# Kernel optimization log

Hardware: AMD Instinct MI355X
Metric: run time of the kernel (lower is better)

The kernel has to match this reference:

```python
import jax, jax.numpy as jnp
import numpy as np

N_NODES = 50000
N_EDGES = 800000


def gcn_conv(x, edge_index, W, b):
    """PyG GCNConv: add self-loops, symmetric deg^{-1/2} normalization,
    dense transform, scatter-add aggregation."""
    n = x.shape[0]
    src, dst = edge_index[0], edge_index[1]
    # add self-loops
    loop = jnp.arange(n, dtype=src.dtype)
    src = jnp.concatenate([src, loop])
    dst = jnp.concatenate([dst, loop])
    # degree on destination nodes (includes self-loops -> deg >= 1)
    deg = jax.ops.segment_sum(jnp.ones_like(dst, dtype=x.dtype), dst, num_segments=n)
    dinv = jax.lax.rsqrt(deg)
    norm = dinv[src] * dinv[dst]  # [E+N]
    h = x @ W                     # [N, F_out] dense GEMM
    msg = h[src] * norm[:, None]  # gather + scale, [E+N, F_out]
    out = jax.ops.segment_sum(msg, dst, num_segments=n)  # scatter-add
    return out + b


def setup_inputs() -> dict:
    key = jax.random.key(0)
    ks = jax.random.split(key, 8)
    x = jax.random.normal(ks[0], (N_NODES, 100), dtype=jnp.float32)
    edge_index = jax.random.randint(ks[1], (2, N_EDGES), 0, N_NODES, dtype=jnp.int64)
    W1 = jax.random.normal(ks[2], (100, 256), dtype=jnp.float32) * 0.1
    b1 = jnp.zeros((256,), dtype=jnp.float32)
    W2 = jax.random.normal(ks[3], (256, 128), dtype=jnp.float32) * 0.06
    b2 = jnp.zeros((128,), dtype=jnp.float32)
    Wfc = jax.random.normal(ks[4], (128, 1), dtype=jnp.float32) * 0.09
    bfc = jnp.zeros((1,), dtype=jnp.float32)
    return {"x": x, "edge_index": edge_index, "W1": W1, "b1": b1,
            "W2": W2, "b2": b2, "Wfc": Wfc, "bfc": bfc}


def reference(x, edge_index, W1, b1, W2, b2, Wfc, bfc):
    # eval mode: F.dropout with training=False is identity
    h = jax.nn.relu(gcn_conv(x, edge_index, W1, b1))
    h = jax.nn.relu(gcn_conv(h, edge_index, W2, b2))
    return h @ Wfc + bfc  # [N, 1]
```

## Files before the change

### kernel.cpp

```cpp
#include <hip/hip_runtime.h>
#include <hip/hip_bf16.h>


#define F0 100
#define F1 256
#define F2 128
#define CAP 2048

typedef _Float16 f16x4 __attribute__((ext_vector_type(4)));
typedef _Float16 f16x8 __attribute__((ext_vector_type(8)));
typedef float f32x4 __attribute__((ext_vector_type(4)));


__global__ void zero_i32(int* p, int n) {
    int i = blockIdx.x * blockDim.x + threadIdx.x;
    if (i < n) p[i] = 0;
}

__global__ void fill_f32(float* out, const float* __restrict__ bfc, int n) {
    int i = blockIdx.x * blockDim.x + threadIdx.x;
    if (i < n) out[i] = bfc[0];
}

__global__ void deg_count_i(const int* __restrict__ dst, int* deg, int e) {
    int i = blockIdx.x * blockDim.x + threadIdx.x;
    if (i < e) atomicAdd(deg + dst[i], 1);
}

__global__ __launch_bounds__(256) void scan1(const int* __restrict__ deg,
                                             int* __restrict__ excl,
                                             int* __restrict__ bsum,
                                             float* __restrict__ dinv, int n) {
    __shared__ int wsum[4];
    int i = blockIdx.x * 256 + threadIdx.x;
    int lane = threadIdx.x & 63, wid = threadIdx.x >> 6;
    int v = (i < n) ? deg[i] : 0;
    if (i < n) dinv[i] = rsqrtf((float)(v + 1));
    int s = v;
#pragma unroll
    for (int off = 1; off < 64; off <<= 1) {
        int t = __shfl_up(s, off, 64);
        if (lane >= off) s += t;
    }
    if (lane == 63) wsum[wid] = s;
    __syncthreads();
    int add = 0;
    for (int w = 0; w < wid; w++) add += wsum[w];
    if (i < n) excl[i] = add + s - v;
    if (threadIdx.x == 255) bsum[blockIdx.x] = add + s;
}

__global__ __launch_bounds__(256) void scan2(int* __restrict__ bsum, int nb,
                                             int* __restrict__ rowptr, int n) {
    __shared__ int wsum[4];
    int lane = threadIdx.x & 63, wid = threadIdx.x >> 6;
    int v = (threadIdx.x < nb) ? bsum[threadIdx.x] : 0;
    int s = v;
#pragma unroll
    for (int off = 1; off < 64; off <<= 1) {
        int t = __shfl_up(s, off, 64);
        if (lane >= off) s += t;
    }
    if (lane == 63) wsum[wid] = s;
    __syncthreads();
    int add = 0;
    for (int w = 0; w < wid; w++) add += wsum[w];
    if (threadIdx.x < nb) bsum[threadIdx.x] = add + s - v;
    if (threadIdx.x == 255) rowptr[n] = add + s;
}

__global__ void scan3(const int* __restrict__ excl, const int* __restrict__ bsum,
                      int* __restrict__ rowptr, int* __restrict__ cursor, int n) {
    int i = blockIdx.x * 256 + threadIdx.x;
    if (i < n) {
        int r = excl[i] + bsum[blockIdx.x];
        rowptr[i] = r;
        cursor[i] = r;
    }
}

__global__ void csr_fill(const int* __restrict__ src, const int* __restrict__ dst,
                         int* cursor, int* __restrict__ csr, int e) {
    int i = blockIdx.x * blockDim.x + threadIdx.x;
    if (i < e) {
        int pos = atomicAdd(cursor + dst[i], 1);
        csr[pos] = src[i];
    }
}

__global__ void scale_x(const float4* __restrict__ x4,
                        const float* __restrict__ dinv,
                        float4* __restrict__ xs4, int n25) {
    int i = blockIdx.x * blockDim.x + threadIdx.x;
    if (i < n25) {
        float d = dinv[i / 25];
        float4 v = x4[i];
        v.x *= d; v.y *= d; v.z *= d; v.w *= d;
        xs4[i] = v;
    }
}

__global__ void wprep(const float* __restrict__ W1, const float* __restrict__ W2,
                      _Float16* __restrict__ W1h, _Float16* __restrict__ W1l,
                      _Float16* __restrict__ W2h, _Float16* __restrict__ W2l) {
    int i = blockIdx.x * 256 + threadIdx.x;
    if (i < 256 * 128) {
        int c = i >> 7, k = i & 127;
        float v = (k < F0) ? W1[(size_t)k * F1 + c] : 0.f;
        _Float16 h = (_Float16)v;
        W1h[i] = h;
        W1l[i] = (_Float16)(v - (float)h);
    } else if (i < 256 * 128 + 128 * 256) {
        int j = i - 256 * 128;
        int c = j >> 8, k = j & 255;
        float v = W2[(size_t)k * F2 + c];
        _Float16 h = (_Float16)v;
        W2h[j] = h;
        W2l[j] = (_Float16)(v - (float)h);
    }
}


__global__ __launch_bounds__(256) void pull_f100(
        const float* __restrict__ xs, const int* __restrict__ rowptr,
        const int* __restrict__ csr, const float* __restrict__ dinv,
        _Float16* __restrict__ aggh, _Float16* __restrict__ aggl, int n) {
    int wave = threadIdx.x >> 6, lane = threadIdx.x & 63;
    int v = blockIdx.x * 4 + wave;
    if (v >= n) return;
    int beg = rowptr[v], end = rowptr[v + 1];
    float dv = dinv[v];
    int half = lane >> 5, q = lane & 31;
    bool act = q < 25;
    float4 acc = {0.f, 0.f, 0.f, 0.f};
    if (half == 0 && act) acc = ((const float4*)(xs + (size_t)v * F0))[q];

    for (int base = beg; base < end; base += 64) {
        int cnt = min(64, end - base);
        int sidx = (lane < cnt) ? csr[base + lane] : 0;
        int npf = cnt >> 1;
        int p = 0;
        for (; p + 4 <= npf; p += 4) {
            int s0 = __shfl(sidx, 2 * p + half, 64);
            int s1 = __shfl(sidx, 2 * p + 2 + half, 64);
            int s2 = __shfl(sidx, 2 * p + 4 + half, 64);
            int s3 = __shfl(sidx, 2 * p + 6 + half, 64);
            if (act) {
                float4 r0 = ((const float4*)(xs + (size_t)s0 * F0))[q];
                float4 r1 = ((const float4*)(xs + (size_t)s1 * F0))[q];
                float4 r2 = ((const float4*)(xs + (size_t)s2 * F0))[q];
                float4 r3 = ((const float4*)(xs + (size_t)s3 * F0))[q];
                acc.x += (r0.x + r1.x) + (r2.x + r3.x);
                acc.y += (r0.y + r1.y) + (r2.y + r3.y);
                acc.z += (r0.z + r1.z) + (r2.z + r3.z);
                acc.w += (r0.w + r1.w) + (r2.w + r3.w);
            }
        }
        for (; p < npf; p++) {
            int s0 = __shfl(sidx, 2 * p + half, 64);
            if (act) {
                float4 r0 = ((const float4*)(xs + (size_t)s0 * F0))[q];
                acc.x += r0.x; acc.y += r0.y; acc.z += r0.z; acc.w += r0.w;
            }
        }
        if (cnt & 1) {
            int sl = __shfl(sidx, cnt - 1, 64);
            if (half == 0 && act) {
                float4 r = ((const float4*)(xs + (size_t)sl * F0))[q];
                acc.x += r.x; acc.y += r.y; acc.z += r.z; acc.w += r.w;
            }
        }
    }
    float ox = __shfl_down(acc.x, 32, 64);
    float oy = __shfl_down(acc.y, 32, 64);
    float oz = __shfl_down(acc.z, 32, 64);
    float ow = __shfl_down(acc.w, 32, 64);
    if (half == 0) {
        float4 r = {0.f, 0.f, 0.f, 0.f};
        if (act) {
            r.x = dv * (acc.x + ox);
            r.y = dv * (acc.y + oy);
            r.z = dv * (acc.z + oz);
            r.w = dv * (acc.w + ow);
        }
        f16x4 hh, ll;
        hh[0] = (_Float16)r.x; ll[0] = (_Float16)(r.x - (float)hh[0]);
        hh[1] = (_Float16)r.y; ll[1] = (_Float16)(r.y - (float)hh[1]);
        hh[2] = (_Float16)r.z; ll[2] = (_Float16)(r.z - (float)hh[2]);
        hh[3] = (_Float16)r.w; ll[3] = (_Float16)(r.w - (float)hh[3]);
        *(f16x4*)(aggh + (size_t)v * 128 + 4 * q) = hh;
        *(f16x4*)(aggl + (size_t)v * 128 + 4 * q) = ll;
    }
}


__global__ __launch_bounds__(256) void gemm1_mfma(
        const _Float16* __restrict__ Ah, const _Float16* __restrict__ Al,
        const _Float16* __restrict__ Bh, const _Float16* __restrict__ Bl,
        const float* __restrict__ bias,
        _Float16* __restrict__ Ch, _Float16* __restrict__ Cl, int n) {
    __shared__ _Float16 sAh[128][40], sAl[128][40], sBh[128][40], sBl[128][40];
    int tid = threadIdx.x, lane = tid & 63, wave = tid >> 6;
    int wm = wave >> 1, wn = wave & 1;
    int r0 = blockIdx.x * 128, c0 = blockIdx.y * 128;
    int lr = lane & 15, ks8 = (lane >> 4) * 8;
    f32x4 acc[4][4] = {};

    for (int k0 = 0; k0 < 128; k0 += 32) {
        if (k0) __syncthreads();
#pragma unroll
        for (int p = 0; p < 2; ++p) {
            int u = tid + p * 256;
            int row = u >> 2, vv = u & 3;
            int gr = min(r0 + row, n - 1);
            *(f16x8*)&sAh[row][vv * 8] = *(const f16x8*)(Ah + (size_t)gr * 128 + k0 + vv * 8);
            *(f16x8*)&sAl[row][vv * 8] = *(const f16x8*)(Al + (size_t)gr * 128 + k0 + vv * 8);
            *(f16x8*)&sBh[row][vv * 8] = *(const f16x8*)(Bh + (size_t)(c0 + row) * 128 + k0 + vv * 8);
            *(f16x8*)&sBl[row][vv * 8] = *(const f16x8*)(Bl + (size_t)(c0 + row) * 128 + k0 + vv * 8);
        }
        __syncthreads();
        f16x8 a_h[4], a_l[4], b_h[4], b_l[4];
#pragma unroll
        for (int f = 0; f < 4; ++f) {
            a_h[f] = *(const f16x8*)&sAh[wm * 64 + f * 16 + lr][ks8];
            a_l[f] = *(const f16x8*)&sAl[wm * 64 + f * 16 + lr][ks8];
            b_h[f] = *(const f16x8*)&sBh[wn * 64 + f * 16 + lr][ks8];
            b_l[f] = *(const f16x8*)&sBl[wn * 64 + f * 16 + lr][ks8];
        }
#pragma unroll
        for (int i = 0; i < 4; ++i)
#pragma unroll
            for (int j = 0; j < 4; ++j) {
                acc[i][j] = __builtin_amdgcn_mfma_f32_16x16x32_f16(a_l[i], b_h[j], acc[i][j], 0, 0, 0);
                acc[i][j] = __builtin_amdgcn_mfma_f32_16x16x32_f16(a_h[i], b_l[j], acc[i][j], 0, 0, 0);
                acc[i][j] = __builtin_amdgcn_mfma_f32_16x16x32_f16(a_h[i], b_h[j], acc[i][j], 0, 0, 0);
            }
    }
#pragma unroll
    for (int j = 0; j < 4; ++j) {
        int col = c0 + wn * 64 + j * 16 + lr;
        float bv = bias[col];
#pragma unroll
        for (int i = 0; i < 4; ++i) {
            int rbase = r0 + wm * 64 + i * 16 + (lane >> 4) * 4;
#pragma unroll
            for (int r = 0; r < 4; ++r) {
                int gr = rbase + r;
                if (gr < n) {
                    float vv = fmaxf(acc[i][j][r] + bv, 0.f);
                    _Float16 h = (_Float16)vv;
                    Ch[(size_t)gr * 256 + col] = h;
                    Cl[(size_t)gr * 256 + col] = (_Float16)(vv - (float)h);
                }
            }
        }
    }
}

__global__ __launch_bounds__(256) void gemm2_mfma(
        const _Float16* __restrict__ Ah, const _Float16* __restrict__ Al,
        const _Float16* __restrict__ Bh, const _Float16* __restrict__ Bl,
        const float* __restrict__ dinv, float* __restrict__ C, int n) {
    __shared__ _Float16 sAh[128][40], sAl[128][40], sBh[128][40], sBl[128][40];
    int tid = threadIdx.x, lane = tid & 63, wave = tid >> 6;
    int wm = wave >> 1, wn = wave & 1;
    int r0 = blockIdx.x * 128;
    int lr = lane & 15, ks8 = (lane >> 4) * 8;
    f32x4 acc[4][4] = {};

    for (int k0 = 0; k0 < 256; k0 += 32) {
        if (k0) __syncthreads();
#pragma unroll
        for (int p = 0; p < 2; ++p) {
            int u = tid + p * 256;
            int row = u >> 2, vv = u & 3;
            int gr = min(r0 + row, n - 1);
            *(f16x8*)&sAh[row][vv * 8] = *(const f16x8*)(Ah + (size_t)gr * 256 + k0 + vv * 8);
            *(f16x8*)&sAl[row][vv * 8] = *(const f16x8*)(Al + (size_t)gr * 256 + k0 + vv * 8);
            *(f16x8*)&sBh[row][vv * 8] = *(const f16x8*)(Bh + (size_t)row * 256 + k0 + vv * 8);
            *(f16x8*)&sBl[row][vv * 8] = *(const f16x8*)(Bl + (size_t)row * 256 + k0 + vv * 8);
        }
        __syncthreads();
        f16x8 a_h[4], a_l[4], b_h[4], b_l[4];
#pragma unroll
        for (int f = 0; f < 4; ++f) {
            a_h[f] = *(const f16x8*)&sAh[wm * 64 + f * 16 + lr][ks8];
            a_l[f] = *(const f16x8*)&sAl[wm * 64 + f * 16 + lr][ks8];
            b_h[f] = *(const f16x8*)&sBh[wn * 64 + f * 16 + lr][ks8];
            b_l[f] = *(const f16x8*)&sBl[wn * 64 + f * 16 + lr][ks8];
        }
#pragma unroll
        for (int i = 0; i < 4; ++i)
#pragma unroll
            for (int j = 0; j < 4; ++j) {
                acc[i][j] = __builtin_amdgcn_mfma_f32_16x16x32_f16(a_l[i], b_h[j], acc[i][j], 0, 0, 0);
                acc[i][j] = __builtin_amdgcn_mfma_f32_16x16x32_f16(a_h[i], b_l[j], acc[i][j], 0, 0, 0);
                acc[i][j] = __builtin_amdgcn_mfma_f32_16x16x32_f16(a_h[i], b_h[j], acc[i][j], 0, 0, 0);
            }
    }
#pragma unroll
    for (int j = 0; j < 4; ++j) {
        int chunk = wn * 4 + j;
#pragma unroll
        for (int i = 0; i < 4; ++i) {
            int rbase = r0 + wm * 64 + i * 16 + (lane >> 4) * 4;
#pragma unroll
            for (int r = 0; r < 4; ++r) {
                int gr = rbase + r;
                if (gr < n) {
                    float d = dinv[gr];
                    C[((size_t)chunk * n + gr) * 16 + lr] = acc[i][j][r] * d;
                }
            }
        }
    }
}


__global__ __launch_bounds__(256) void pull_c16_fused(
        const float* __restrict__ h2c, const int* __restrict__ rowptr,
        const int* __restrict__ csr, const float* __restrict__ dinv,
        const float* __restrict__ b2, const float* __restrict__ Wfc,
        float* __restrict__ out, int n) {
    __shared__ int s_row[65];
    __shared__ float s_dinv[64];
    __shared__ int s_csr[CAP];
    int chunk = blockIdx.x & 7;
    int nb = blockIdx.x >> 3;
    int v0 = nb * 64;
    int tid = threadIdx.x;
    int lane = tid & 63, wv = tid >> 6;
    int q = lane & 3;
    int g2 = (lane >> 2) & 3;
    int grp = lane >> 4;
    const float* __restrict__ tab = h2c + (size_t)chunk * n * 16;

    if (tid <= 64) s_row[tid] = rowptr[min(v0 + tid, n)];
    if (tid < 64) s_dinv[tid] = (v0 + tid < n) ? dinv[v0 + tid] : 0.f;
    __syncthreads();
    int ebeg = s_row[0], eend = s_row[64];

    int base_local = wv * 16 + grp * 4;

    float4 acc[4];
#pragma unroll
    for (int nn = 0; nn < 4; ++nn) acc[nn] = (float4){0.f, 0.f, 0.f, 0.f};

#pragma unroll
    for (int nn = 0; nn < 4; ++nn) {
        int node = v0 + base_local + nn;
        if (node < n && g2 == 0)
            acc[nn] = ((const float4*)(tab + (size_t)node * 16))[q];
    }

    for (int w0 = ebeg; w0 < eend; w0 += CAP) {
        int wcnt = min(CAP, eend - w0);
        if (w0 != ebeg) __syncthreads();
        for (int i = tid; i < wcnt; i += 256)
            s_csr[i] = __builtin_nontemporal_load(csr + w0 + i);
        __syncthreads();
#pragma unroll
        for (int nn = 0; nn < 4; ++nn) {
            int local = base_local + nn;
            int nbg = max(s_row[local], w0) - w0;
            int nen = min(s_row[local + 1], w0 + wcnt) - w0;
            for (int t = nbg + 4 * g2; t < nen; t += 16) {
                int i1 = min(t + 1, nen - 1);
                int i2 = min(t + 2, nen - 1);
                int i3 = min(t + 3, nen - 1);
                int s0 = s_csr[t];
                int s1 = s_csr[i1];
                int s2 = s_csr[i2];
                int s3 = s_csr[i3];
                float4 r0 = ((const float4*)(tab + (size_t)s0 * 16))[q];
                float4 r1 = ((const float4*)(tab + (size_t)s1 * 16))[q];
                float4 r2 = ((const float4*)(tab + (size_t)s2 * 16))[q];
                float4 r3 = ((const float4*)(tab + (size_t)s3 * 16))[q];
                bool m1 = (t + 1 < nen), m2 = (t + 2 < nen), m3 = (t + 3 < nen);
                acc[nn].x += r0.x + (m1 ? r1.x : 0.f);
                acc[nn].y += r0.y + (m1 ? r1.y : 0.f);
                acc[nn].z += r0.z + (m1 ? r1.z : 0.f);
                acc[nn].w += r0.w + (m1 ? r1.w : 0.f);
                acc[nn].x += (m2 ? r2.x : 0.f) + (m3 ? r3.x : 0.f);
                acc[nn].y += (m2 ? r2.y : 0.f) + (m3 ? r3.y : 0.f);
                acc[nn].z += (m2 ? r2.z : 0.f) + (m3 ? r3.z : 0.f);
                acc[nn].w += (m2 ? r2.w : 0.f) + (m3 ? r3.w : 0.f);
            }
        }
    }

    int c0 = chunk * 16 + 4 * q;
    float4 bb = *(const float4*)(b2 + c0);
    float4 ww = *(const float4*)(Wfc + c0);
#pragma unroll
    for (int nn = 0; nn < 4; ++nn) {
        int local = base_local + nn;
        int node = v0 + local;
        float dv = s_dinv[local];
        float4 a = acc[nn];
        a.x += __shfl_xor(a.x, 4, 64);
        a.y += __shfl_xor(a.y, 4, 64);
        a.z += __shfl_xor(a.z, 4, 64);
        a.w += __shfl_xor(a.w, 4, 64);
        a.x += __shfl_xor(a.x, 8, 64);
        a.y += __shfl_xor(a.y, 8, 64);
        a.z += __shfl_xor(a.z, 8, 64);
        a.w += __shfl_xor(a.w, 8, 64);
        float part = fmaxf(fmaf(dv, a.x, bb.x), 0.f) * ww.x
                   + fmaxf(fmaf(dv, a.y, bb.y), 0.f) * ww.y
                   + fmaxf(fmaf(dv, a.z, bb.z), 0.f) * ww.z
                   + fmaxf(fmaf(dv, a.w, bb.w), 0.f) * ww.w;
        part += __shfl_xor(part, 1, 64);
        part += __shfl_xor(part, 2, 64);
        if (node < n && (lane & 15) == 0) atomicAdd(out + node, part);
    }
}


extern "C" void kernel_launch(void* const* d_in, const int* in_sizes, int n_in,
                              void* d_out, int out_size, void* d_ws, size_t ws_size,
                              hipStream_t stream) {
    const float* x   = (const float*)d_in[0];
    const int*   ei  = (const int*)d_in[1];
    const float* W1  = (const float*)d_in[2];
    const float* b1  = (const float*)d_in[3];
    const float* W2  = (const float*)d_in[4];
    const float* b2  = (const float*)d_in[5];
    const float* Wfc = (const float*)d_in[6];
    const float* bfc = (const float*)d_in[7];
    float* out = (float*)d_out;

    const int n = in_sizes[0] / F0;
    const int e = in_sizes[1] / 2;
    const int* src = ei;
    const int* dst = ei + e;

    char* wsb = (char*)d_ws;
    size_t off = 0;
    auto alloc = [&](size_t bytes) -> void* {
        off = (off + 255) & ~(size_t)255;
        void* r = wsb + off;
        off += bytes;
        return r;
    };
    int* deg    = (int*)alloc((size_t)n * 4);
    int* excl   = (int*)alloc((size_t)n * 4);
    int* bsum   = (int*)alloc(1024);
    int* rowptr = (int*)alloc((size_t)(n + 1) * 4);
    int* cursor = (int*)alloc((size_t)n * 4);
    int* csr    = (int*)alloc((size_t)e * 4);
    float* dinv = (float*)alloc((size_t)n * 4);
    _Float16* W1h = (_Float16*)alloc(256 * 128 * 2);
    _Float16* W1l = (_Float16*)alloc(256 * 128 * 2);
    _Float16* W2h = (_Float16*)alloc(128 * 256 * 2);
    _Float16* W2l = (_Float16*)alloc(128 * 256 * 2);
    char* bufA = (char*)alloc((size_t)n * 256 * 2 * 2);
    float* xs = (float*)bufA;
    _Float16* a1h = (_Float16*)bufA;
    _Float16* a1l = a1h + (size_t)n * 256;
    char* bufB = (char*)alloc((size_t)n * 128 * 4);
    _Float16* aggh = (_Float16*)bufB;
    _Float16* aggl = aggh + (size_t)n * 128;
    float* h2c = (float*)bufB;

    const int B = 256;
    const int nb = (n + B - 1) / B;
    const int rblocks = (n + 127) / 128;

    zero_i32<<<nb, B, 0, stream>>>(deg, n);
    fill_f32<<<nb, B, 0, stream>>>(out, bfc, n);
    deg_count_i<<<(e + B - 1) / B, B, 0, stream>>>(dst, deg, e);
    scan1<<<nb, B, 0, stream>>>(deg, excl, bsum, dinv, n);
    scale_x<<<((n * 25) + B - 1) / B, B, 0, stream>>>(
        (const float4*)x, dinv, (float4*)xs, n * 25);
    wprep<<<256, 256, 0, stream>>>(W1, W2, W1h, W1l, W2h, W2l);
    scan2<<<1, B, 0, stream>>>(bsum, nb, rowptr, n);
    scan3<<<nb, B, 0, stream>>>(excl, bsum, rowptr, cursor, n);
    csr_fill<<<(e + B - 1) / B, B, 0, stream>>>(src, dst, cursor, csr, e);

    pull_f100<<<(n + 3) / 4, 256, 0, stream>>>(xs, rowptr, csr, dinv, aggh, aggl, n);
    gemm1_mfma<<<dim3(rblocks, 2), 256, 0, stream>>>(aggh, aggl, W1h, W1l, b1,
                                                     a1h, a1l, n);
    gemm2_mfma<<<rblocks, 256, 0, stream>>>(a1h, a1l, W2h, W2l, dinv, h2c, n);
    pull_c16_fused<<<8 * ((n + 63) / 64), 256, 0, stream>>>(
        h2c, rowptr, csr, dinv, b2, Wfc, out, n);
}
```

Measured before the change: 346.6 us.

## Fuse layer-1 and layer-2 GEMMs into one kernel keeping hidden tile in LDS

Merges the two MFMA GEMMs into a single 512-thread kernel. Each block computes its 128-row slice of the 256-wide hidden activation in registers, applies bias and ReLU, and stages the split-fp16 result in LDS in two halves, which feed the second GEMM directly. This removes the global write and re-read of the n×256 hi/lo intermediate and one launch. The first GEMM now reads A and W1 straight from global memory without LDS staging, and the two-half staging adds barriers. The grid shrinks to one block per 128 rows (about 391 blocks of 512 threads), and the large register and LDS footprint may cut occupancy.

```diff
diff --git a/kernel.cpp b/kernel.cpp
--- a/kernel.cpp
+++ b/kernel.cpp
@@ -193,127 +193,117 @@
     }
 }
 
-
-__global__ __launch_bounds__(256) void gemm1_mfma(
+__global__ __launch_bounds__(512) void gemm12_fused(
         const _Float16* __restrict__ Ah, const _Float16* __restrict__ Al,
-        const _Float16* __restrict__ Bh, const _Float16* __restrict__ Bl,
-        const float* __restrict__ bias,
-        _Float16* __restrict__ Ch, _Float16* __restrict__ Cl, int n) {
-    __shared__ _Float16 sAh[128][40], sAl[128][40], sBh[128][40], sBl[128][40];
+        const _Float16* __restrict__ W1h, const _Float16* __restrict__ W1l,
+        const _Float16* __restrict__ W2h, const _Float16* __restrict__ W2l,
+        const float* __restrict__ b1, const float* __restrict__ dinv,
+        float* __restrict__ C, int n) {
+    __shared__ _Float16 sAh[128][136], sAl[128][136];
     int tid = threadIdx.x, lane = tid & 63, wave = tid >> 6;
-    int wm = wave >> 1, wn = wave & 1;
-    int r0 = blockIdx.x * 128, c0 = blockIdx.y * 128;
-    int lr = lane & 15, ks8 = (lane >> 4) * 8;
-    f32x4 acc[4][4] = {};
-
+    int wm = wave >> 2, wn = wave & 3;
+    int r0 = blockIdx.x * 128;
+    int lr = lane & 15, kg = lane >> 4, ks8 = kg * 8;
+
+    f32x4 acc1[4][4] = {};
+    int arow[4];
+#pragma unroll
+    for (int i = 0; i < 4; ++i) arow[i] = min(r0 + wm * 64 + i * 16 + lr, n - 1);
+
+#pragma unroll
     for (int k0 = 0; k0 < 128; k0 += 32) {
-        if (k0) __syncthreads();
-#pragma unroll
-        for (int p = 0; p < 2; ++p) {
-            int u = tid + p * 256;
-            int row = u >> 2, vv = u & 3;
-            int gr = min(r0 + row, n - 1);
-            *(f16x8*)&sAh[row][vv * 8] = *(const f16x8*)(Ah + (size_t)gr * 128 + k0 + vv * 8);
-            *(f16x8*)&sAl[row][vv * 8] = *(const f16x8*)(Al + (size_t)gr * 128 + k0 + vv * 8);
-            *(f16x8*)&sBh[row][vv * 8] = *(const f16x8*)(Bh + (size_t)(c0 + row) * 128 + k0 + vv * 8);
-            *(f16x8*)&sBl[row][vv * 8] = *(const f16x8*)(Bl + (size_t)(c0 + row) * 128 + k0 + vv * 8);
+        f16x8 a_h[4], a_l[4], b_h[4], b_l[4];
+#pragma unroll
+        for (int i = 0; i < 4; ++i) {
+            a_h[i] = *(const f16x8*)(Ah + (size_t)arow[i] * 128 + k0 + ks8);
+            a_l[i] = *(const f16x8*)(Al + (size_t)arow[i] * 128 + k0 + ks8);
+        }
+#pragma unroll
+        for (int j = 0; j < 4; ++j) {
+            int col = wn * 64 + j * 16 + lr;
+            b_h[j] = *(const f16x8*)(W1h + (size_t)col * 128 + k0 + ks8);
+            b_l[j] = *(const f16x8*)(W1l + (size_t)col * 128 + k0 + ks8);
+        }
+#pragma unroll
+        for (int i = 0; i < 4; ++i)
+#pragma unroll
+            for (int j = 0; j < 4; ++j) {
+                acc1[i][j] = __builtin_amdgcn_mfma_f32_16x16x32_f16(a_l[i], b_h[j], acc1[i][j], 0, 0, 0);
+                acc1[i][j] = __builtin_amdgcn_mfma_f32_16x16x32_f16(a_h[i], b_l[j], acc1[i][j], 0, 0, 0);
+                acc1[i][j] = __builtin_amdgcn_mfma_f32_16x16x32_f16(a_h[i], b_h[j], acc1[i][j], 0, 0, 0);
+            }
+    }
+#pragma unroll
+    for (int j = 0; j < 4; ++j) {
+        float bv = b1[wn * 64 + j * 16 + lr];
+#pragma unroll
+        for (int i = 0; i < 4; ++i)
+#pragma unroll
+            for (int r = 0; r < 4; ++r)
+                acc1[i][j][r] = fmaxf(acc1[i][j][r] + bv, 0.f);
+    }
+
+    f32x4 acc2[4][2] = {};
+#pragma unroll
+    for (int half = 0; half < 2; ++half) {
+        if (half) __syncthreads();
+        if ((wn >> 1) == half) {
+            int cb = (wn & 1) * 64;
+#pragma unroll
+            for (int i = 0; i < 4; ++i)
+#pragma unroll
+                for (int j = 0; j < 4; ++j)
+#pragma unroll
+                    for (int r = 0; r < 4; ++r) {
+                        int row = wm * 64 + i * 16 + kg * 4 + r;
+                        int col = cb + j * 16 + lr;
+                        float v = acc1[i][j][r];
+                        _Float16 h = (_Float16)v;
+                        sAh[row][col] = h;
+                        sAl[row][col] = (_Float16)(v - (float)h);
+                    }
         }
         __syncthreads();
-        f16x8 a_h[4], a_l[4], b_h[4], b_l[4];
-#pragma unroll
-        for (int f = 0; f < 4; ++f) {
-            a_h[f] = *(const f16x8*)&sAh[wm * 64 + f * 16 + lr][ks8];
-            a_l[f] = *(const f16x8*)&sAl[wm * 64 + f * 16 + lr][ks8];
-            b_h[f] = *(const f16x8*)&sBh[wn * 64 + f * 16 + lr][ks8];
-            b_l[f] = *(const f16x8*)&sBl[wn * 64 + f * 16 + lr][ks8];
-        }
-#pragma unroll
-        for (int i = 0; i < 4; ++i)
-#pragma unroll
-            for (int j = 0; j < 4; ++j) {
-                acc[i][j] = __builtin_amdgcn_mfma_f32_16x16x32_f16(a_l[i], b_h[j], acc[i][j], 0, 0, 0);
-                acc[i][j] = __builtin_amdgcn_mfma_f32_16x16x32_f16(a_h[i], b_l[j], acc[i][j], 0, 0, 0);
-                acc[i][j] = __builtin_amdgcn_mfma_f32_16x16x32_f16(a_h[i], b_h[j], acc[i][j], 0, 0, 0);
-            }
-    }
-#pragma unroll
-    for (int j = 0; j < 4; ++j) {
-        int col = c0 + wn * 64 + j * 16 + lr;
-        float bv = bias[col];
-#pragma unroll
-        for (int i = 0; i < 4; ++i) {
-            int rbase = r0 + wm * 64 + i * 16 + (lane >> 4) * 4;
-#pragma unroll
-            for (int r = 0; r < 4; ++r) {
-                int gr = rbase + r;
-                if (gr < n) {
-                    float vv = fmaxf(acc[i][j][r] + bv, 0.f);
-                    _Float16 h = (_Float16)vv;
-                    Ch[(size_t)gr * 256 + col] = h;
-                    Cl[(size_t)gr * 256 + col] = (_Float16)(vv - (float)h);
+#pragma unroll
+        for (int k0 = 0; k0 < 128; k0 += 32) {
+            f16x8 a_h[4], a_l[4], b_h[2], b_l[2];
+#pragma unroll
+            for (int i = 0; i < 4; ++i) {
+                a_h[i] = *(const f16x8*)&sAh[wm * 64 + i * 16 + lr][k0 + ks8];
+                a_l[i] = *(const f16x8*)&sAl[wm * 64 + i * 16 + lr][k0 + ks8];
+            }
+#pragma unroll
+            for (int j = 0; j < 2; ++j) {
+                int col = wn * 32 + j * 16 + lr;
+                int kk = half * 128 + k0 + ks8;
+                b_h[j] = *(const f16x8*)(W2h + (size_t)col * 256 + kk);
+                b_l[j] = *(const f16x8*)(W2l + (size_t)col * 256 + kk);
+            }
+#pragma unroll
+            for (int i = 0; i < 4; ++i)
+#pragma unroll
+                for (int j = 0; j < 2; ++j) {
+                    acc2[i][j] = __builtin_amdgcn_mfma_f32_16x16x32_f16(a_l[i], b_h[j], acc2[i][j], 0, 0, 0);
+                    acc2[i][j] = __builtin_amdgcn_mfma_f32_16x16x32_f16(a_h[i], b_l[j], acc2[i][j], 0, 0, 0);
+                    acc2[i][j] = __builtin_amdgcn_mfma_f32_16x16x32_f16(a_h[i], b_h[j], acc2[i][j], 0, 0, 0);
                 }
-            }
-        }
-    }
-}
-
-__global__ __launch_bounds__(256) void gemm2_mfma(
-        const _Float16* __restrict__ Ah, const _Float16* __restrict__ Al,
-        const _Float16* __restrict__ Bh, const _Float16* __restrict__ Bl,
-        const float* __restrict__ dinv, float* __restrict__ C, int n) {
-    __shared__ _Float16 sAh[128][40], sAl[128][40], sBh[128][40], sBl[128][40];
-    int tid = threadIdx.x, lane = tid & 63, wave = tid >> 6;
-    int wm = wave >> 1, wn = wave & 1;
-    int r0 = blockIdx.x * 128;
-    int lr = lane & 15, ks8 = (lane >> 4) * 8;
-    f32x4 acc[4][4] = {};
-
-    for (int k0 = 0; k0 < 256; k0 += 32) {
-        if (k0) __syncthreads();
-#pragma unroll
-        for (int p = 0; p < 2; ++p) {
-            int u = tid + p * 256;
-            int row = u >> 2, vv = u & 3;
-            int gr = min(r0 + row, n - 1);
-            *(f16x8*)&sAh[row][vv * 8] = *(const f16x8*)(Ah + (size_t)gr * 256 + k0 + vv * 8);
-            *(f16x8*)&sAl[row][vv * 8] = *(const f16x8*)(Al + (size_t)gr * 256 + k0 + vv * 8);
-            *(f16x8*)&sBh[row][vv * 8] = *(const f16x8*)(Bh + (size_t)row * 256 + k0 + vv * 8);
-            *(f16x8*)&sBl[row][vv * 8] = *(const f16x8*)(Bl + (size_t)row * 256 + k0 + vv * 8);
-        }
-        __syncthreads();
-        f16x8 a_h[4], a_l[4], b_h[4], b_l[4];
-#pragma unroll
-        for (int f = 0; f < 4; ++f) {
-            a_h[f] = *(const f16x8*)&sAh[wm * 64 + f * 16 + lr][ks8];
-            a_l[f] = *(const f16x8*)&sAl[wm * 64 + f * 16 + lr][ks8];
-            b_h[f] = *(const f16x8*)&sBh[wn * 64 + f * 16 + lr][ks8];
-            b_l[f] = *(const f16x8*)&sBl[wn * 64 + f * 16 + lr][ks8];
-        }
-#pragma unroll
-        for (int i = 0; i < 4; ++i)
-#pragma unroll
-            for (int j = 0; j < 4; ++j) {
-                acc[i][j] = __builtin_amdgcn_mfma_f32_16x16x32_f16(a_l[i], b_h[j], acc[i][j], 0, 0, 0);
-                acc[i][j] = __builtin_amdgcn_mfma_f32_16x16x32_f16(a_h[i], b_l[j], acc[i][j], 0, 0, 0);
-                acc[i][j] = __builtin_amdgcn_mfma_f32_16x16x32_f16(a_h[i], b_h[j], acc[i][j], 0, 0, 0);
-            }
-    }
-#pragma unroll
-    for (int j = 0; j < 4; ++j) {
-        int chunk = wn * 4 + j;
-#pragma unroll
-        for (int i = 0; i < 4; ++i) {
-            int rbase = r0 + wm * 64 + i * 16 + (lane >> 4) * 4;
-#pragma unroll
-            for (int r = 0; r < 4; ++r) {
-                int gr = rbase + r;
-                if (gr < n) {
-                    float d = dinv[gr];
-                    C[((size_t)chunk * n + gr) * 16 + lr] = acc[i][j][r] * d;
+        }
+    }
+
+#pragma unroll
+    for (int i = 0; i < 4; ++i)
+#pragma unroll
+        for (int r = 0; r < 4; ++r) {
+            int gr = r0 + wm * 64 + i * 16 + kg * 4 + r;
+            if (gr < n) {
+                float d = dinv[gr];
+#pragma unroll
+                for (int j = 0; j < 2; ++j) {
+                    int chunk = wn * 2 + j;
+                    C[((size_t)chunk * n + gr) * 16 + lr] = acc2[i][j][r] * d;
                 }
             }
         }
-    }
 }
 
 
@@ -454,14 +444,11 @@
     _Float16* W1l = (_Float16*)alloc(256 * 128 * 2);
     _Float16* W2h = (_Float16*)alloc(128 * 256 * 2);
     _Float16* W2l = (_Float16*)alloc(128 * 256 * 2);
-    char* bufA = (char*)alloc((size_t)n * 256 * 2 * 2);
-    float* xs = (float*)bufA;
-    _Float16* a1h = (_Float16*)bufA;
-    _Float16* a1l = a1h + (size_t)n * 256;
-    char* bufB = (char*)alloc((size_t)n * 128 * 4);
-    _Float16* aggh = (_Float16*)bufB;
-    _Float16* aggl = aggh + (size_t)n * 128;
-    float* h2c = (float*)bufB;
+    char* bufA = (char*)alloc((size_t)n * 128 * 4);
+    float* xs  = (float*)bufA;
+    float* h2c = (float*)bufA;
+    _Float16* aggh = (_Float16*)alloc((size_t)n * 128 * 2);
+    _Float16* aggl = (_Float16*)alloc((size_t)n * 128 * 2);
 
     const int B = 256;
     const int nb = (n + B - 1) / B;
@@ -479,9 +466,8 @@
     csr_fill<<<(e + B - 1) / B, B, 0, stream>>>(src, dst, cursor, csr, e);
 
     pull_f100<<<(n + 3) / 4, 256, 0, stream>>>(xs, rowptr, csr, dinv, aggh, aggl, n);
-    gemm1_mfma<<<dim3(rblocks, 2), 256, 0, stream>>>(aggh, aggl, W1h, W1l, b1,
-                                                     a1h, a1l, n);
-    gemm2_mfma<<<rblocks, 256, 0, stream>>>(a1h, a1l, W2h, W2l, dinv, h2c, n);
+    gemm12_fused<<<rblocks, 512, 0, stream>>>(aggh, aggl, W1h, W1l, W2h, W2l,
+                                              b1, dinv, h2c, n);
     pull_c16_fused<<<8 * ((n + 63) / 64), 256, 0, stream>>>(
         h2c, rowptr, csr, dinv, b2, Wfc, out, n);
 }
```

New measurement: 343.5 us. About the same (-0.9%).
